# Performance work log

Measured on AMD Instinct MI355X. Metric: run time of the kernel, lower is better.

The kernel has to match this reference:

```python
import jax, jax.numpy as jnp
import numpy as np

H, DH, DM = 8, 128, 1024          # n_head, d_head, d_model (n_head*d_head == d_model)
SLEN, BSZ = 256, 64               # slen <= 256 forced by pi0[:, :l]
SCALE = 1.0 / DH ** 0.5
LN_EPS = 1e-5


def setup_inputs() -> dict:
    key = jax.random.key(0)
    k0, k1, k2, k3 = jax.random.split(key, 4)
    h = jax.random.normal(k0, (SLEN, BSZ, DM), jnp.float32)
    W_qkv = jax.random.normal(k1, (H * 4 * DH, DM), jnp.float32) * (DM ** -0.5)
    W_o = jax.random.normal(k2, (DM, H * DH), jnp.float32) * ((H * DH) ** -0.5)
    pi0 = jax.random.uniform(k3, (H, 256), jnp.float32)
    ln_gamma = jnp.ones((DM,), jnp.float32)
    ln_beta = jnp.zeros((DM,), jnp.float32)
    return {"h": h, "W_qkv": W_qkv, "W_o": W_o, "pi0": pi0,
            "ln_gamma": ln_gamma, "ln_beta": ln_beta}


def _phi(x):
    # elu(x)+1 feature map, then L1-normalize over the feature dim
    x = jax.nn.elu(x) + 1.0
    return x / jnp.sum(x, axis=-1, keepdims=True)


def _causal_linear_attn(q, k, v):
    # fast_weight_sum: out_t = sum_{s<=t} (q_t . k_s) v_s  (zero initial fast weights)
    # q,k,v: [b,h,l,d]
    l = q.shape[2]
    scores = jnp.einsum('bhld,bhsd->bhls', q, k)
    mask = jnp.tril(jnp.ones((l, l), dtype=bool))
    scores = jnp.where(mask, scores, jnp.zeros((), scores.dtype))
    return jnp.einsum('bhls,bhsd->bhld', scores, v)


def reference(h, W_qkv, W_o, pi0, ln_gamma, ln_beta):
    l, b, _ = h.shape
    # qkv projection: [l,b,H,4*DH] -> q, k1, k2, v (update_mode='rbf2keys')
    qkv = jnp.einsum('lbm,nm->lbn', h, W_qkv).reshape(l, b, H, 4 * DH)
    q, k1, k2, v = jnp.split(qkv, 4, axis=-1)
    # permute to [b, H, l, d]
    q = _phi(jnp.transpose(q, (1, 2, 0, 3)))
    k1 = _phi(jnp.transpose(k1, (1, 2, 0, 3)))
    k2 = _phi(jnp.transpose(k2, (1, 2, 0, 3)))
    v = jnp.transpose(v, (1, 2, 0, 3))
    # two fast-weight sums (skip_attn_normalization=True path)
    lo1 = _causal_linear_attn(q, k1, v)
    lo2 = _causal_linear_attn(q, k2, v)
    pi = jnp.clip(pi0, 0.0, 1.0)[None, :, :l, None]          # [1,H,l,1]
    layer_out = SCALE * (lo1 * pi + lo2 * (1.0 - pi))         # [b,H,l,d]
    # [b,H,l,d] -> [l,b,H*d]
    layer_out = jnp.transpose(layer_out, (2, 0, 1, 3)).reshape(l, b, H * DH)
    attn_out = jnp.einsum('lbn,mn->lbm', layer_out, W_o)
    # post-LN residual (pre_lnorm=False, dropout=0)
    x = h + attn_out
    mu = jnp.mean(x, axis=-1, keepdims=True)
    var = jnp.mean((x - mu) ** 2, axis=-1, keepdims=True)
    return ln_gamma * (x - mu) / jnp.sqrt(var + LN_EPS) + ln_beta
```

## Files before the change

kernel.cpp:

```cpp
#include <hip/hip_runtime.h>

#define H_     8
#define DM_    1024
#define NQKV_  4096
#define ROWS_  16384
#define PAIRS_ 512
#define SCALE_ 0.08838834764831845f
#define LN_EPS_ 1e-5f

typedef __attribute__((ext_vector_type(8))) short short8;
typedef __attribute__((ext_vector_type(4))) float floatx4;

__device__ __forceinline__ float b2f(unsigned short u) {
  union { unsigned int i; float f; } v; v.i = ((unsigned int)u) << 16; return v.f;
}
__device__ __forceinline__ unsigned short f2b(float f) {
  union { unsigned int i; float f; } v; v.f = f;
  unsigned int b = v.i;
  b += 0x7FFFu + ((b >> 16) & 1u);
  return (unsigned short)(b >> 16);
}

__device__ __forceinline__ void stage_async(const unsigned short* __restrict__ g,
                                            size_t ld, unsigned short* s, int tid) {
#pragma unroll
  for (int p = 0; p < 4; ++p) {
    int idx = p * 256 + tid;
    int r = idx >> 3, j = idx & 7;
    int cg = j ^ (r & 7);
    __builtin_amdgcn_global_load_lds(
        (const __attribute__((address_space(1))) unsigned int*)(g + (size_t)r * ld + cg * 8),
        (__attribute__((address_space(3))) unsigned int*)(s + (size_t)idx * 8),
        16, 0, 0);
  }
}
__device__ __forceinline__ void stage_h(const unsigned short* __restrict__ g,
                                        size_t o0, size_t o1,
                                        unsigned short* s, int lo0, int lo1) {
  __builtin_amdgcn_global_load_lds(
      (const __attribute__((address_space(1))) unsigned int*)(g + o0),
      (__attribute__((address_space(3))) unsigned int*)(s + lo0), 16, 0, 0);
  __builtin_amdgcn_global_load_lds(
      (const __attribute__((address_space(1))) unsigned int*)(g + o1),
      (__attribute__((address_space(3))) unsigned int*)(s + lo1), 16, 0, 0);
}
__device__ __forceinline__ short8 lds_frag(const unsigned short* s, int row, int cg) {
  return *(const short8*)(s + row * 64 + ((cg ^ (row & 7)) << 3));
}

__global__ __launch_bounds__(256) void cvt_all(const float* __restrict__ h,
                                               const float* __restrict__ wq,
                                               const float* __restrict__ wo,
                                               unsigned short* __restrict__ hb,
                                               unsigned short* __restrict__ wqb,
                                               unsigned short* __restrict__ wob) {
  int i = blockIdx.x * 256 + threadIdx.x;
  const float* src; unsigned short* dst; int off;
  if (i < 2097152)      { src = h;  dst = hb;  off = i; }
  else if (i < 2621440) { src = wq; dst = wqb; off = i - 2097152; }
  else                  { src = wo; dst = wob; off = i - 2621440; }
  const float4* s4 = (const float4*)(src + (size_t)off * 8);
  float4 v0 = s4[0], v1 = s4[1];
  union { short8 v; unsigned short u[8]; } pk;
  pk.u[0] = f2b(v0.x); pk.u[1] = f2b(v0.y); pk.u[2] = f2b(v0.z); pk.u[3] = f2b(v0.w);
  pk.u[4] = f2b(v1.x); pk.u[5] = f2b(v1.y); pk.u[6] = f2b(v1.z); pk.u[7] = f2b(v1.w);
  *(short8*)(dst + (size_t)off * 8) = pk.v;
}

__global__ __launch_bounds__(512, 2) void qkv_gemm(const unsigned short* __restrict__ A,
                                                   const unsigned short* __restrict__ B,
                                                   unsigned short* __restrict__ QKV) {
  __shared__ alignas(16) unsigned short Sh[65536];
  int tid = threadIdx.x;
  int lane = tid & 63, wid = tid >> 6;
  int wm = wid >> 2, wn = wid & 3;
  int quad = lane >> 4, l16 = lane & 15;
  int s7 = l16 & 7;

  int bid = blockIdx.y * 16 + blockIdx.x;
  int swz = (bid & 7) * 128 + (bid >> 3);
  int bx = swz & 15, by = swz >> 4;
  int n0 = bx * 256, hh = bx >> 1, part0 = (bx & 1) * 2, bb = by;

  const unsigned short* Ab = A + (size_t)bb * DM_;
  const size_t lda = (size_t)64 * DM_;
  const unsigned short* AbH = Ab + (size_t)128 * lda;
  const unsigned short* Bb = B + (size_t)n0 * DM_;
  const unsigned short* BbH = Bb + (size_t)128 * DM_;

  int r0 = tid >> 3, jj = tid & 7;
  int cg = jj ^ (r0 & 7);
  size_t oA0 = (size_t)r0 * lda + cg * 8;
  size_t oA1 = (size_t)(r0 + 64) * lda + cg * 8;
  size_t oB0 = (size_t)r0 * DM_ + cg * 8;
  size_t oB1 = (size_t)(r0 + 64) * DM_ + cg * 8;
  int lo0 = tid * 8, lo1 = 4096 + tid * 8;

  floatx4 acc[8][4];
#pragma unroll
  for (int i = 0; i < 8; ++i)
#pragma unroll
    for (int j = 0; j < 4; ++j)
#pragma unroll
      for (int r = 0; r < 4; ++r) acc[i][j][r] = 0.f;

  stage_h(Ab,        oA0, oA1, Sh,         lo0, lo1);
  stage_h(AbH,       oA0, oA1, Sh + 8192,  lo0, lo1);
  stage_h(Bb,        oB0, oB1, Sh + 16384, lo0, lo1);
  stage_h(BbH,       oB0, oB1, Sh + 24576, lo0, lo1);
  stage_h(Ab + 64,   oA0, oA1, Sh + 32768, lo0, lo1);
  stage_h(AbH + 64,  oA0, oA1, Sh + 40960, lo0, lo1);
  asm volatile("s_waitcnt vmcnt(4)" ::: "memory");
  __builtin_amdgcn_s_barrier();

#define TILE_BODY(T, BUF, OBUF)                                                \
  {                                                                            \
    unsigned short* SB = (BUF) + 16384;                                        \
    const unsigned short* aA0 = (BUF) + (wm * 128 + l16) * 64 + ((0 ^ (quad ^ s7)) ? 0 : 0) + ((quad ^ s7) << 3); \
    const unsigned short* aA1 = (BUF) + (wm * 128 + l16) * 64 + (((4 + quad) ^ s7) << 3); \
    const unsigned short* bA0 = SB + (wn * 64 + l16) * 64 + ((quad ^ s7) << 3);\
    const unsigned short* bA1 = SB + (wn * 64 + l16) * 64 + (((4 + quad) ^ s7) << 3); \
    short8 a[8], b[4];                                                         \
                   \
    if ((T) < 15) {                                                            \
      size_t kn = (size_t)((T) + 1) * 64;                                      \
      stage_h(Bb + kn,  oB0, oB1, (OBUF) + 16384, lo0, lo1);                   \
      stage_h(BbH + kn, oB0, oB1, (OBUF) + 24576, lo0, lo1);                   \
    }                                                                          \
    _Pragma("unroll")                                                          \
    for (int mt = 0; mt < 4; ++mt) {                                           \
      a[mt * 2 + 0] = *(const short8*)(aA0 + mt * 1024);                       \
      a[mt * 2 + 1] = *(const short8*)(aA1 + mt * 1024);                       \
    }                                                                          \
    _Pragma("unroll")                                                          \
    for (int nt = 0; nt < 2; ++nt) {                                           \
      b[nt * 2 + 0] = *(const short8*)(bA0 + nt * 1024);                       \
      b[nt * 2 + 1] = *(const short8*)(bA1 + nt * 1024);                       \
    }                                                                          \
    __builtin_amdgcn_sched_barrier(0);                                         \
    __builtin_amdgcn_s_barrier();                                              \
    __builtin_amdgcn_s_setprio(1);                                             \
    _Pragma("unroll")                                                          \
    for (int kk = 0; kk < 2; ++kk)                                             \
      _Pragma("unroll")                                                        \
      for (int m = 0; m < 4; ++m)                                              \
        _Pragma("unroll")                                                      \
        for (int n = 0; n < 2; ++n)                                            \
          acc[m][n] = __builtin_amdgcn_mfma_f32_16x16x32_bf16(a[m * 2 + kk], b[n * 2 + kk], acc[m][n], 0, 0, 0); \
    __builtin_amdgcn_s_setprio(0);                                             \
    __builtin_amdgcn_s_barrier();                                              \
                                                 \
    _Pragma("unroll")                                                          \
    for (int nt = 0; nt < 2; ++nt) {                                           \
      b[nt * 2 + 0] = *(const short8*)(bA0 + 2048 + nt * 1024);                \
      b[nt * 2 + 1] = *(const short8*)(bA1 + 2048 + nt * 1024);                \
    }                                                                          \
    __builtin_amdgcn_sched_barrier(0);                                         \
    __builtin_amdgcn_s_barrier();                                              \
    __builtin_amdgcn_s_setprio(1);                                             \
    _Pragma("unroll")                                                          \
    for (int kk = 0; kk < 2; ++kk)                                             \
      _Pragma("unroll")                                                        \
      for (int m = 0; m < 4; ++m)                                              \
        _Pragma("unroll")                                                      \
        for (int n = 0; n < 2; ++n)                                            \
          acc[m][2 + n] = __builtin_amdgcn_mfma_f32_16x16x32_bf16(a[m * 2 + kk], b[n * 2 + kk], acc[m][2 + n], 0, 0, 0); \
    __builtin_amdgcn_s_setprio(0);                                             \
    __builtin_amdgcn_s_barrier();                                              \
                                       \
    _Pragma("unroll")                                                          \
    for (int mt = 0; mt < 4; ++mt) {                                           \
      a[mt * 2 + 0] = *(const short8*)(aA0 + 4096 + mt * 1024);                \
      a[mt * 2 + 1] = *(const short8*)(aA1 + 4096 + mt * 1024);                \
    }                                                                          \
    __builtin_amdgcn_sched_barrier(0);                                         \
    __builtin_amdgcn_s_barrier();                                              \
    __builtin_amdgcn_s_setprio(1);                                             \
    _Pragma("unroll")                                                          \
    for (int kk = 0; kk < 2; ++kk)                                             \
      _Pragma("unroll")                                                        \
      for (int m = 0; m < 4; ++m)                                              \
        _Pragma("unroll")                                                      \
        for (int n = 0; n < 2; ++n)                                            \
          acc[4 + m][2 + n] = __builtin_amdgcn_mfma_f32_16x16x32_bf16(a[m * 2 + kk], b[n * 2 + kk], acc[4 + m][2 + n], 0, 0, 0); \
    __builtin_amdgcn_s_setprio(0);                                             \
    __builtin_amdgcn_s_barrier();                                              \
                \
    if ((T) < 14) {                                                            \
      size_t kt2 = (size_t)((T) + 2) * 64;                                     \
      stage_h(Ab + kt2,  oA0, oA1, (BUF),        lo0, lo1);                    \
      stage_h(AbH + kt2, oA0, oA1, (BUF) + 8192, lo0, lo1);                    \
    }                                                                          \
    _Pragma("unroll")                                                          \
    for (int nt = 0; nt < 2; ++nt) {                                           \
      b[nt * 2 + 0] = *(const short8*)(bA0 + nt * 1024);                       \
      b[nt * 2 + 1] = *(const short8*)(bA1 + nt * 1024);                       \
    }                                                                          \
    __builtin_amdgcn_sched_barrier(0);                                         \
    __builtin_amdgcn_s_barrier();                                              \
    __builtin_amdgcn_s_setprio(1);                                             \
    _Pragma("unroll")                                                          \
    for (int kk = 0; kk < 2; ++kk)                                             \
      _Pragma("unroll")                                                        \
      for (int m = 0; m < 4; ++m)                                              \
        _Pragma("unroll")                                                      \
        for (int n = 0; n < 2; ++n)                                            \
          acc[4 + m][n] = __builtin_amdgcn_mfma_f32_16x16x32_bf16(a[m * 2 + kk], b[n * 2 + kk], acc[4 + m][n], 0, 0, 0); \
    __builtin_amdgcn_s_setprio(0);                                             \
    if ((T) < 14) { asm volatile("s_waitcnt vmcnt(4)" ::: "memory"); }         \
    else          { asm volatile("s_waitcnt vmcnt(0)" ::: "memory"); }         \
    __builtin_amdgcn_s_barrier();                                              \
  }

  for (int t = 0; t < 16; t += 2) {
    TILE_BODY(t,     Sh,         Sh + 32768)
    TILE_BODY(t + 1, Sh + 32768, Sh)
  }
#undef TILE_BODY

  __syncthreads();
  bool isV = (part0 + (wn >> 1)) == 3;
  float* Pf = (float*)Sh;
  float rsum[8][4];
  float inv[8][4];
  if (!isV) {
#pragma unroll
    for (int mt = 0; mt < 8; ++mt)
#pragma unroll
      for (int r = 0; r < 4; ++r) rsum[mt][r] = 0.f;
#pragma unroll
    for (int mt = 0; mt < 8; ++mt)
#pragma unroll
      for (int nt = 0; nt < 4; ++nt)
#pragma unroll
        for (int r = 0; r < 4; ++r) {
          float x = acc[mt][nt][r];
          float f = x > 0.f ? x + 1.f : __expf(x);
          acc[mt][nt][r] = f;
          rsum[mt][r] += f;
        }
#pragma unroll
    for (int off = 1; off < 16; off <<= 1)
#pragma unroll
      for (int mt = 0; mt < 8; ++mt)
#pragma unroll
        for (int r = 0; r < 4; ++r)
          rsum[mt][r] += __shfl_xor(rsum[mt][r], off);
    if (l16 == 0) {
#pragma unroll
      for (int mt = 0; mt < 8; ++mt)
#pragma unroll
        for (int r = 0; r < 4; ++r)
          Pf[(wm * 128 + mt * 16 + quad * 4 + r) * 4 + wn] = rsum[mt][r];
    }
  }
  __syncthreads();
  if (!isV) {
#pragma unroll
    for (int mt = 0; mt < 8; ++mt)
#pragma unroll
      for (int r = 0; r < 4; ++r)
        inv[mt][r] = 1.f / (rsum[mt][r] + Pf[(wm * 128 + mt * 16 + quad * 4 + r) * 4 + (wn ^ 1)]);
  }
  __syncthreads();

#pragma unroll
  for (int h = 0; h < 2; ++h) {
    int part = part0 + h;
    if ((wn >> 1) == h) {
      if (part < 3) {
#pragma unroll
        for (int mt = 0; mt < 8; ++mt)
#pragma unroll
          for (int nt = 0; nt < 4; ++nt)
#pragma unroll
            for (int r = 0; r < 4; ++r) {
              int row = wm * 128 + mt * 16 + quad * 4 + r;
              int col = (wn & 1) * 64 + nt * 16 + l16;
              Sh[row * 136 + col] = f2b(acc[mt][nt][r] * inv[mt][r]);
            }
      } else {
#pragma unroll
        for (int mt = 0; mt < 8; ++mt)
#pragma unroll
          for (int nt = 0; nt < 4; ++nt)
#pragma unroll
            for (int r = 0; r < 4; ++r) {
              int d = (wn & 1) * 64 + nt * 16 + l16;
              int l = wm * 128 + mt * 16 + quad * 4 + r;
              Sh[d * 264 + l] = f2b(acc[mt][nt][r]);
            }
      }
    }
    __syncthreads();
    if (part < 3) {
      unsigned short* P = QKV + (size_t)part * 16777216 + (size_t)(bb * 8 + hh) * 32768;
      int c = tid & 15, g = tid >> 4;
#pragma unroll
      for (int j = 0; j < 8; ++j) {
        int row = j * 32 + g;
        *(short8*)(P + (size_t)row * 128 + c * 8) = *(const short8*)(Sh + row * 136 + c * 8);
      }
    } else {
      unsigned short* Vt = QKV + (size_t)3 * 16777216 + (size_t)(bb * 8 + hh) * 32768;
      int cg2 = tid & 31, g = tid >> 5;
#pragma unroll
      for (int j = 0; j < 8; ++j) {
        int d = j * 16 + g;
        *(short8*)(Vt + (size_t)d * 256 + cg2 * 8) = *(const short8*)(Sh + d * 264 + cg2 * 8);
      }
    }
    __syncthreads();
  }
}

__global__ __launch_bounds__(256) void scores_kernel(const unsigned short* __restrict__ QKV,
                                                     const float* __restrict__ pi0,
                                                     unsigned short* __restrict__ S) {
  __shared__ alignas(16) unsigned short Sh[24576];
  __shared__ float pis[128];
  unsigned short* As  = Sh;
  unsigned short* Bs1 = Sh + 8192;
  unsigned short* Bs2 = Sh + 16384;
  int p = blockIdx.z;
  int hh = p & 7;
  int tid = threadIdx.x;
  int lane = tid & 63, wid = tid >> 6;
  int wm = wid >> 1, wn = wid & 1;
  int quad = lane >> 4, l16 = lane & 15;
  int tix = blockIdx.x;
  int m0 = (tix >= 1) ? 128 : 0;
  int n0 = (tix == 2) ? 128 : 0;
  if (tid < 128) {
    float pv = pi0[hh * 256 + m0 + tid];
    pis[tid] = fminf(fmaxf(pv, 0.f), 1.f);
  }
  const unsigned short* Qb  = QKV + (size_t)p * 32768 + (size_t)m0 * 128;
  const unsigned short* K1b = QKV + 16777216     + (size_t)p * 32768 + (size_t)n0 * 128;
  const unsigned short* K2b = QKV + 2 * 16777216 + (size_t)p * 32768 + (size_t)n0 * 128;

  floatx4 acc1[4][4], acc2[4][4];
#pragma unroll
  for (int i = 0; i < 4; ++i)
#pragma unroll
    for (int j = 0; j < 4; ++j)
#pragma unroll
      for (int r = 0; r < 4; ++r) { acc1[i][j][r] = 0.f; acc2[i][j][r] = 0.f; }

  for (int kt = 0; kt < 128; kt += 64) {
    stage_async(Qb + kt, 128, As, tid);
    stage_async(K1b + kt, 128, Bs1, tid);
    stage_async(K2b + kt, 128, Bs2, tid);
    __syncthreads();
#pragma unroll
    for (int kk = 0; kk < 2; ++kk) {
      short8 af[4], b1[4], b2v[4];
#pragma unroll
      for (int mt = 0; mt < 4; ++mt)
        af[mt] = lds_frag(As, wm * 64 + mt * 16 + l16, kk * 4 + quad);
#pragma unroll
      for (int nt = 0; nt < 4; ++nt) {
        b1[nt]  = lds_frag(Bs1, wn * 64 + nt * 16 + l16, kk * 4 + quad);
        b2v[nt] = lds_frag(Bs2, wn * 64 + nt * 16 + l16, kk * 4 + quad);
      }
#pragma unroll
      for (int mt = 0; mt < 4; ++mt)
#pragma unroll
        for (int nt = 0; nt < 4; ++nt) {
          acc1[mt][nt] = __builtin_amdgcn_mfma_f32_16x16x32_bf16(af[mt], b1[nt],  acc1[mt][nt], 0, 0, 0);
          acc2[mt][nt] = __builtin_amdgcn_mfma_f32_16x16x32_bf16(af[mt], b2v[nt], acc2[mt][nt], 0, 0, 0);
        }
    }
    __syncthreads();
  }
#pragma unroll
  for (int mt = 0; mt < 4; ++mt)
#pragma unroll
    for (int nt = 0; nt < 4; ++nt)
#pragma unroll
      for (int r = 0; r < 4; ++r) {
        int tl = wm * 64 + mt * 16 + quad * 4 + r;
        int sl = wn * 64 + nt * 16 + l16;
        float pv = pis[tl];
        float v = (n0 + sl <= m0 + tl) ? (pv * acc1[mt][nt][r] + (1.f - pv) * acc2[mt][nt][r]) : 0.f;
        Sh[tl * 136 + sl] = f2b(v);
      }
  __syncthreads();
  int c = tid & 15, g = tid >> 4;
#pragma unroll
  for (int j = 0; j < 8; ++j) {
    int r = j * 16 + g;
    size_t gb = (size_t)p * 65536 + (size_t)(m0 + r) * 256 + n0 + c * 8;
    *(short8*)(S + gb) = *(const short8*)(Sh + r * 136 + c * 8);
  }
}

__global__ __launch_bounds__(256, 4) void pv_kernel(const unsigned short* __restrict__ S,
                                                    const unsigned short* __restrict__ Vt,
                                                    unsigned short* __restrict__ LO) {
  __shared__ alignas(16) unsigned short Sh[17408];
  unsigned short* As = Sh;
  unsigned short* Bs = Sh + 8192;
  int p = blockIdx.z;
  int b = p >> 3, hh = p & 7;
  int tid = threadIdx.x;
  int lane = tid & 63, wid = tid >> 6;
  int wm = wid >> 1, wn = wid & 1;
  int quad = lane >> 4, l16 = lane & 15;
  int m0 = blockIdx.y * 128;
  int kEnd = (blockIdx.y == 0) ? 128 : 256;
  const unsigned short* Ab = S  + (size_t)p * 65536 + (size_t)m0 * 256;
  const unsigned short* Bb = Vt + (size_t)p * 32768;

  floatx4 acc[4][4];
#pragma unroll
  for (int i = 0; i < 4; ++i)
#pragma unroll
    for (int j = 0; j < 4; ++j)
#pragma unroll
      for (int r = 0; r < 4; ++r) acc[i][j][r] = 0.f;

  for (int kt = 0; kt < kEnd; kt += 64) {
    stage_async(Ab + kt, 256, As, tid);
    stage_async(Bb + kt, 256, Bs, tid);
    __syncthreads();
#pragma unroll
    for (int kk = 0; kk < 2; ++kk) {
      short8 af[4], bfv[4];
#pragma unroll
      for (int mt = 0; mt < 4; ++mt)
        af[mt] = lds_frag(As, wm * 64 + mt * 16 + l16, kk * 4 + quad);
#pragma unroll
      for (int nt = 0; nt < 4; ++nt)
        bfv[nt] = lds_frag(Bs, wn * 64 + nt * 16 + l16, kk * 4 + quad);
#pragma unroll
      for (int mt = 0; mt < 4; ++mt)
#pragma unroll
        for (int nt = 0; nt < 4; ++nt)
          acc[mt][nt] = __builtin_amdgcn_mfma_f32_16x16x32_bf16(af[mt], bfv[nt], acc[mt][nt], 0, 0, 0);
    }
    __syncthreads();
  }
#pragma unroll
  for (int mt = 0; mt < 4; ++mt)
#pragma unroll
    for (int nt = 0; nt < 4; ++nt)
#pragma unroll
      for (int r = 0; r < 4; ++r) {
        int tl = wm * 64 + mt * 16 + quad * 4 + r;
        int d = wn * 64 + nt * 16 + l16;
        Sh[tl * 136 + d] = f2b(SCALE_ * acc[mt][nt][r]);
      }
  __syncthreads();
  int c = tid & 15, g = tid >> 4;
#pragma unroll
  for (int j = 0; j < 8; ++j) {
    int r = j * 16 + g;
    int t = m0 + r;
    size_t gb = ((size_t)t * 64 + b) * 1024 + hh * 128 + c * 8;
    *(short8*)(LO + gb) = *(const short8*)(Sh + r * 136 + c * 8);
  }
}

__global__ __launch_bounds__(256, 4) void wo_gemm(const unsigned short* __restrict__ A,
                                                  const unsigned short* __restrict__ B,
                                                  const float* __restrict__ hin,
                                                  float* __restrict__ X) {
  __shared__ alignas(16) unsigned short As[128 * 64], Bs[128 * 64];
  int tid = threadIdx.x;
  int lane = tid & 63, wid = tid >> 6;
  int wm = wid >> 1, wn = wid & 1;
  int quad = lane >> 4, l16 = lane & 15;
  int m0 = blockIdx.y * 128, n0 = blockIdx.x * 128;
  const unsigned short* Ab = A + (size_t)m0 * DM_;
  const unsigned short* Bb = B + (size_t)n0 * DM_;

  floatx4 acc[4][4];
#pragma unroll
  for (int i = 0; i < 4; ++i)
#pragma unroll
    for (int j = 0; j < 4; ++j)
#pragma unroll
      for (int r = 0; r < 4; ++r) acc[i][j][r] = 0.f;

  for (int kt = 0; kt < DM_; kt += 64) {
    stage_async(Ab + kt, DM_, As, tid);
    stage_async(Bb + kt, DM_, Bs, tid);
    __syncthreads();
#pragma unroll
    for (int kk = 0; kk < 2; ++kk) {
      short8 af[4], bfv[4];
#pragma unroll
      for (int mt = 0; mt < 4; ++mt)
        af[mt] = lds_frag(As, wm * 64 + mt * 16 + l16, kk * 4 + quad);
#pragma unroll
      for (int nt = 0; nt < 4; ++nt)
        bfv[nt] = lds_frag(Bs, wn * 64 + nt * 16 + l16, kk * 4 + quad);
#pragma unroll
      for (int mt = 0; mt < 4; ++mt)
#pragma unroll
        for (int nt = 0; nt < 4; ++nt)
          acc[mt][nt] = __builtin_amdgcn_mfma_f32_16x16x32_bf16(af[mt], bfv[nt], acc[mt][nt], 0, 0, 0);
    }
    __syncthreads();
  }
#pragma unroll
  for (int mt = 0; mt < 4; ++mt)
#pragma unroll
    for (int nt = 0; nt < 4; ++nt)
#pragma unroll
      for (int r = 0; r < 4; ++r) {
        int row = m0 + wm * 64 + mt * 16 + quad * 4 + r;
        int col = n0 + wn * 64 + nt * 16 + l16;
        size_t idx = (size_t)row * DM_ + col;
        X[idx] = acc[mt][nt][r] + hin[idx];
      }
}

__global__ __launch_bounds__(256) void ln_kernel(float* __restrict__ X,
                                                 const float* __restrict__ gamma,
                                                 const float* __restrict__ beta) {
  int row = blockIdx.x;
  int tid = threadIdx.x;
  float* x = X + (size_t)row * DM_;
  float4 v = *(const float4*)(x + tid * 4);
  float s  = v.x + v.y + v.z + v.w;
  float ss = v.x * v.x + v.y * v.y + v.z * v.z + v.w * v.w;
#pragma unroll
  for (int off = 32; off; off >>= 1) {
    s  += __shfl_down(s, off);
    ss += __shfl_down(ss, off);
  }
  __shared__ float rs[4], rss[4];
  int wv = tid >> 6, lane = tid & 63;
  if (lane == 0) { rs[wv] = s; rss[wv] = ss; }
  __syncthreads();
  float St  = rs[0] + rs[1] + rs[2] + rs[3];
  float SSt = rss[0] + rss[1] + rss[2] + rss[3];
  float mu = St * (1.f / DM_);
  float var = SSt * (1.f / DM_) - mu * mu;
  float rstd = rsqrtf(var + LN_EPS_);
  float4 o;
#pragma unroll
  for (int j = 0; j < 4; ++j) {
    int c = tid * 4 + j;
    (&o.x)[j] = gamma[c] * ((&v.x)[j] - mu) * rstd + beta[c];
  }
  *(float4*)(x + tid * 4) = o;
}

extern "C" void kernel_launch(void* const* d_in, const int* in_sizes, int n_in,
                              void* d_out, int out_size, void* d_ws, size_t ws_size,
                              hipStream_t stream) {
  const float* h     = (const float*)d_in[0];
  const float* Wqkv  = (const float*)d_in[1];
  const float* Wo    = (const float*)d_in[2];
  const float* pi0   = (const float*)d_in[3];
  const float* gamma = (const float*)d_in[4];
  const float* beta  = (const float*)d_in[5];
  char* ws = (char*)d_ws;

  unsigned short* QKV   = (unsigned short*)ws;
  unsigned short* Sbuf  = (unsigned short*)(ws + 134217728ull);
  unsigned short* hb    = (unsigned short*)(ws + 134217728ull);
  unsigned short* Wqkvb = (unsigned short*)(ws + 167772160ull);
  unsigned short* Wob   = (unsigned short*)(ws + 201326592ull);
  unsigned short* LO    = (unsigned short*)ws;
  float* X = (float*)d_out;

  dim3 blk(256);
  cvt_all<<<dim3(10752), blk, 0, stream>>>(h, Wqkv, Wo, hb, Wqkvb, Wob);
  qkv_gemm<<<dim3(16, 64, 1), dim3(512), 0, stream>>>(hb, Wqkvb, QKV);
  scores_kernel<<<dim3(3, 1, PAIRS_), blk, 0, stream>>>(QKV, pi0, Sbuf);
  pv_kernel<<<dim3(1, 2, PAIRS_), blk, 0, stream>>>(Sbuf, QKV + (size_t)3 * 16777216, LO);
  wo_gemm<<<dim3(DM_ / 128, ROWS_ / 128, 1), blk, 0, stream>>>(LO, Wob, h, X);
  ln_kernel<<<dim3(ROWS_, 1, 1), blk, 0, stream>>>(X, gamma, beta);
}
```

Baseline: 438.7 us.

## Fuse scores and PV kernels into one attention kernel keeping scores in LDS

Replaces the separate scores and PV kernels with one attn_kernel. Each block computes the mixed, causally masked score panels for its query tile and keeps them in swizzled shared memory, then multiplies them by V without writing S to global memory. This removes the global round trip for the score matrix and one launch. The cost is more shared memory per block (80 KB), serial work in the second query tile, and only 2 blocks per query pair. The qkv_gemm launch bound is also relaxed to one block per SM.

After: 466.0 us. +6.2%, slower.

```diff
diff --git a/kernel.cpp b/kernel.cpp
--- a/kernel.cpp
+++ b/kernel.cpp
@@ -67,7 +67,7 @@
   *(short8*)(dst + (size_t)off * 8) = pk.v;
 }
 
-__global__ __launch_bounds__(512, 2) void qkv_gemm(const unsigned short* __restrict__ A,
+__global__ __launch_bounds__(512, 1) void qkv_gemm(const unsigned short* __restrict__ A,
                                                    const unsigned short* __restrict__ B,
                                                    unsigned short* __restrict__ QKV) {
   __shared__ alignas(16) unsigned short Sh[65536];
@@ -116,7 +116,7 @@
 #define TILE_BODY(T, BUF, OBUF)                                                \
   {                                                                            \
     unsigned short* SB = (BUF) + 16384;                                        \
-    const unsigned short* aA0 = (BUF) + (wm * 128 + l16) * 64 + ((0 ^ (quad ^ s7)) ? 0 : 0) + ((quad ^ s7) << 3); \
+    const unsigned short* aA0 = (BUF) + (wm * 128 + l16) * 64 + ((quad ^ s7) << 3); \
     const unsigned short* aA1 = (BUF) + (wm * 128 + l16) * 64 + (((4 + quad) ^ s7) << 3); \
     const unsigned short* bA0 = SB + (wn * 64 + l16) * 64 + ((quad ^ s7) << 3);\
     const unsigned short* bA1 = SB + (wn * 64 + l16) * 64 + (((4 + quad) ^ s7) << 3); \
@@ -314,103 +314,82 @@
   }
 }
 
-__global__ __launch_bounds__(256) void scores_kernel(const unsigned short* __restrict__ QKV,
-                                                     const float* __restrict__ pi0,
-                                                     unsigned short* __restrict__ S) {
-  __shared__ alignas(16) unsigned short Sh[24576];
-  __shared__ float pis[128];
-  unsigned short* As  = Sh;
-  unsigned short* Bs1 = Sh + 8192;
-  unsigned short* Bs2 = Sh + 16384;
+__global__ __launch_bounds__(256, 2) void attn_kernel(const unsigned short* __restrict__ QKV,
+                                                      const float* __restrict__ pi0,
+                                                      unsigned short* __restrict__ LO) {
+  __shared__ alignas(16) unsigned short Stg[24576];
+  __shared__ alignas(16) unsigned short Span[16384];
+  unsigned short* As  = Stg;
+  unsigned short* Bs1 = Stg + 8192;
+  unsigned short* Bs2 = Stg + 16384;
   int p = blockIdx.z;
-  int hh = p & 7;
+  int b = p >> 3, hh = p & 7;
+  int mi = blockIdx.x;
+  int m0 = mi * 128;
   int tid = threadIdx.x;
   int lane = tid & 63, wid = tid >> 6;
   int wm = wid >> 1, wn = wid & 1;
   int quad = lane >> 4, l16 = lane & 15;
-  int tix = blockIdx.x;
-  int m0 = (tix >= 1) ? 128 : 0;
-  int n0 = (tix == 2) ? 128 : 0;
-  if (tid < 128) {
-    float pv = pi0[hh * 256 + m0 + tid];
-    pis[tid] = fminf(fmaxf(pv, 0.f), 1.f);
-  }
-  const unsigned short* Qb  = QKV + (size_t)p * 32768 + (size_t)m0 * 128;
-  const unsigned short* K1b = QKV + 16777216     + (size_t)p * 32768 + (size_t)n0 * 128;
-  const unsigned short* K2b = QKV + 2 * 16777216 + (size_t)p * 32768 + (size_t)n0 * 128;
-
-  floatx4 acc1[4][4], acc2[4][4];
-#pragma unroll
-  for (int i = 0; i < 4; ++i)
-#pragma unroll
-    for (int j = 0; j < 4; ++j)
-#pragma unroll
-      for (int r = 0; r < 4; ++r) { acc1[i][j][r] = 0.f; acc2[i][j][r] = 0.f; }
-
-  for (int kt = 0; kt < 128; kt += 64) {
-    stage_async(Qb + kt, 128, As, tid);
-    stage_async(K1b + kt, 128, Bs1, tid);
-    stage_async(K2b + kt, 128, Bs2, tid);
-    __syncthreads();
-#pragma unroll
-    for (int kk = 0; kk < 2; ++kk) {
-      short8 af[4], b1[4], b2v[4];
-#pragma unroll
-      for (int mt = 0; mt < 4; ++mt)
-        af[mt] = lds_frag(As, wm * 64 + mt * 16 + l16, kk * 4 + quad);
-#pragma unroll
-      for (int nt = 0; nt < 4; ++nt) {
-        b1[nt]  = lds_frag(Bs1, wn * 64 + nt * 16 + l16, kk * 4 + quad);
-        b2v[nt] = lds_frag(Bs2, wn * 64 + nt * 16 + l16, kk * 4 + quad);
-      }
-#pragma unroll
-      for (int mt = 0; mt < 4; ++mt)
+
+  const unsigned short* Qb = QKV + (size_t)p * 32768 + (size_t)m0 * 128;
+
+  for (int nb = 0; nb <= mi; ++nb) {
+    int n0 = nb * 128;
+    const unsigned short* K1b = QKV + 16777216     + (size_t)p * 32768 + (size_t)n0 * 128;
+    const unsigned short* K2b = QKV + 2 * 16777216 + (size_t)p * 32768 + (size_t)n0 * 128;
+
+    floatx4 acc1[4][4], acc2[4][4];
+#pragma unroll
+    for (int i = 0; i < 4; ++i)
+#pragma unroll
+      for (int j = 0; j < 4; ++j)
+#pragma unroll
+        for (int r = 0; r < 4; ++r) { acc1[i][j][r] = 0.f; acc2[i][j][r] = 0.f; }
+
+    for (int kt = 0; kt < 128; kt += 64) {
+      stage_async(Qb + kt, 128, As, tid);
+      stage_async(K1b + kt, 128, Bs1, tid);
+      stage_async(K2b + kt, 128, Bs2, tid);
+      __syncthreads();
+#pragma unroll
+      for (int kk = 0; kk < 2; ++kk) {
+        short8 af[4], b1[4], b2v[4];
+#pragma unroll
+        for (int mt = 0; mt < 4; ++mt)
+          af[mt] = lds_frag(As, wm * 64 + mt * 16 + l16, kk * 4 + quad);
 #pragma unroll
         for (int nt = 0; nt < 4; ++nt) {
-          acc1[mt][nt] = __builtin_amdgcn_mfma_f32_16x16x32_bf16(af[mt], b1[nt],  acc1[mt][nt], 0, 0, 0);
-          acc2[mt][nt] = __builtin_amdgcn_mfma_f32_16x16x32_bf16(af[mt], b2v[nt], acc2[mt][nt], 0, 0, 0);
+          b1[nt]  = lds_frag(Bs1, wn * 64 + nt * 16 + l16, kk * 4 + quad);
+          b2v[nt] = lds_frag(Bs2, wn * 64 + nt * 16 + l16, kk * 4 + quad);
         }
+#pragma unroll
+        for (int mt = 0; mt < 4; ++mt)
+#pragma unroll
+          for (int nt = 0; nt < 4; ++nt) {
+            acc1[mt][nt] = __builtin_amdgcn_mfma_f32_16x16x32_bf16(af[mt], b1[nt],  acc1[mt][nt], 0, 0, 0);
+            acc2[mt][nt] = __builtin_amdgcn_mfma_f32_16x16x32_bf16(af[mt], b2v[nt], acc2[mt][nt], 0, 0, 0);
+          }
+      }
+      __syncthreads();
     }
-    __syncthreads();
-  }
-#pragma unroll
-  for (int mt = 0; mt < 4; ++mt)
-#pragma unroll
-    for (int nt = 0; nt < 4; ++nt)
+    bool diag = (nb == mi);
+    unsigned short* Pan = Span + (size_t)(nb * 2 + wn) * 8192;
+#pragma unroll
+    for (int mt = 0; mt < 4; ++mt)
 #pragma unroll
       for (int r = 0; r < 4; ++r) {
         int tl = wm * 64 + mt * 16 + quad * 4 + r;
-        int sl = wn * 64 + nt * 16 + l16;
-        float pv = pis[tl];
-        float v = (n0 + sl <= m0 + tl) ? (pv * acc1[mt][nt][r] + (1.f - pv) * acc2[mt][nt][r]) : 0.f;
-        Sh[tl * 136 + sl] = f2b(v);
-      }
-  __syncthreads();
-  int c = tid & 15, g = tid >> 4;
-#pragma unroll
-  for (int j = 0; j < 8; ++j) {
-    int r = j * 16 + g;
-    size_t gb = (size_t)p * 65536 + (size_t)(m0 + r) * 256 + n0 + c * 8;
-    *(short8*)(S + gb) = *(const short8*)(Sh + r * 136 + c * 8);
-  }
-}
-
-__global__ __launch_bounds__(256, 4) void pv_kernel(const unsigned short* __restrict__ S,
-                                                    const unsigned short* __restrict__ Vt,
-                                                    unsigned short* __restrict__ LO) {
-  __shared__ alignas(16) unsigned short Sh[17408];
-  unsigned short* As = Sh;
-  unsigned short* Bs = Sh + 8192;
-  int p = blockIdx.z;
-  int b = p >> 3, hh = p & 7;
-  int tid = threadIdx.x;
-  int lane = tid & 63, wid = tid >> 6;
-  int wm = wid >> 1, wn = wid & 1;
-  int quad = lane >> 4, l16 = lane & 15;
-  int m0 = blockIdx.y * 128;
-  int kEnd = (blockIdx.y == 0) ? 128 : 256;
-  const unsigned short* Ab = S  + (size_t)p * 65536 + (size_t)m0 * 256;
-  const unsigned short* Bb = Vt + (size_t)p * 32768;
+        float pv = pi0[hh * 256 + m0 + tl];
+        pv = fminf(fmaxf(pv, 0.f), 1.f);
+#pragma unroll
+        for (int nt = 0; nt < 4; ++nt) {
+          int slc = nt * 16 + l16;
+          float v = pv * acc1[mt][nt][r] + (1.f - pv) * acc2[mt][nt][r];
+          if (diag && (n0 + wn * 64 + slc > m0 + tl)) v = 0.f;
+          Pan[tl * 64 + (((slc >> 3) ^ (tl & 7)) << 3) + (slc & 7)] = f2b(v);
+        }
+      }
+  }
 
   floatx4 acc[4][4];
 #pragma unroll
@@ -420,19 +399,21 @@
 #pragma unroll
       for (int r = 0; r < 4; ++r) acc[i][j][r] = 0.f;
 
+  int kEnd = m0 + 128;
+  const unsigned short* Vb = QKV + (size_t)3 * 16777216 + (size_t)p * 32768;
   for (int kt = 0; kt < kEnd; kt += 64) {
-    stage_async(Ab + kt, 256, As, tid);
-    stage_async(Bb + kt, 256, Bs, tid);
+    stage_async(Vb + kt, 256, Bs1, tid);
     __syncthreads();
+    const unsigned short* Ap = Span + (size_t)(kt >> 6) * 8192;
 #pragma unroll
     for (int kk = 0; kk < 2; ++kk) {
       short8 af[4], bfv[4];
 #pragma unroll
       for (int mt = 0; mt < 4; ++mt)
-        af[mt] = lds_frag(As, wm * 64 + mt * 16 + l16, kk * 4 + quad);
+        af[mt] = lds_frag(Ap, wm * 64 + mt * 16 + l16, kk * 4 + quad);
 #pragma unroll
       for (int nt = 0; nt < 4; ++nt)
-        bfv[nt] = lds_frag(Bs, wn * 64 + nt * 16 + l16, kk * 4 + quad);
+        bfv[nt] = lds_frag(Bs1, wn * 64 + nt * 16 + l16, kk * 4 + quad);
 #pragma unroll
       for (int mt = 0; mt < 4; ++mt)
 #pragma unroll
@@ -441,6 +422,7 @@
     }
     __syncthreads();
   }
+
 #pragma unroll
   for (int mt = 0; mt < 4; ++mt)
 #pragma unroll
@@ -449,7 +431,9 @@
       for (int r = 0; r < 4; ++r) {
         int tl = wm * 64 + mt * 16 + quad * 4 + r;
         int d = wn * 64 + nt * 16 + l16;
-        Sh[tl * 136 + d] = f2b(SCALE_ * acc[mt][nt][r]);
+        int dc = d & 63;
+        Span[(size_t)(d >> 6) * 8192 + tl * 64 + (((dc >> 3) ^ (tl & 7)) << 3) + (dc & 7)] =
+            f2b(SCALE_ * acc[mt][nt][r]);
       }
   __syncthreads();
   int c = tid & 15, g = tid >> 4;
@@ -457,8 +441,9 @@
   for (int j = 0; j < 8; ++j) {
     int r = j * 16 + g;
     int t = m0 + r;
+    short8 val = *(const short8*)(Span + (size_t)(c >> 3) * 8192 + r * 64 + (((c & 7) ^ (r & 7)) << 3));
     size_t gb = ((size_t)t * 64 + b) * 1024 + hh * 128 + c * 8;
-    *(short8*)(LO + gb) = *(const short8*)(Sh + r * 136 + c * 8);
+    *(short8*)(LO + gb) = val;
   }
 }
 
@@ -561,18 +546,16 @@
   char* ws = (char*)d_ws;
 
   unsigned short* QKV   = (unsigned short*)ws;
-  unsigned short* Sbuf  = (unsigned short*)(ws + 134217728ull);
   unsigned short* hb    = (unsigned short*)(ws + 134217728ull);
   unsigned short* Wqkvb = (unsigned short*)(ws + 167772160ull);
   unsigned short* Wob   = (unsigned short*)(ws + 201326592ull);
-  unsigned short* LO    = (unsigned short*)ws;
+  unsigned short* LO    = (unsigned short*)(ws + 134217728ull);
   float* X = (float*)d_out;
 
   dim3 blk(256);
   cvt_all<<<dim3(10752), blk, 0, stream>>>(h, Wqkv, Wo, hb, Wqkvb, Wob);
   qkv_gemm<<<dim3(16, 64, 1), dim3(512), 0, stream>>>(hb, Wqkvb, QKV);
-  scores_kernel<<<dim3(3, 1, PAIRS_), blk, 0, stream>>>(QKV, pi0, Sbuf);
-  pv_kernel<<<dim3(1, 2, PAIRS_), blk, 0, stream>>>(Sbuf, QKV + (size_t)3 * 16777216, LO);
+  attn_kernel<<<dim3(2, 1, PAIRS_), blk, 0, stream>>>(QKV, pi0, LO);
   wo_gemm<<<dim3(DM_ / 128, ROWS_ / 128, 1), blk, 0, stream>>>(LO, Wob, h, X);
   ln_kernel<<<dim3(ROWS_, 1, 1), blk, 0, stream>>>(X, gamma, beta);
 }
```

## Reuse pipelined 256x256 qkv GEMM tile for Wo projection, fuse residual into LN

Applied to the files above, without the earlier changes.

The Wo GEMM now reuses the double-buffered, swizzled 256x256 TILE_BODY pipeline from the QKV GEMM instead of a simple 128x128 synchronous loop. It writes a bf16 attention output through an LDS-staged coalesced store. The residual add moves into a new ln_res kernel that reads bf16 attn plus fp32 h. This is meant to raise GEMM efficiency and cut fp32 X write/read traffic, at the cost of rounding attn_out to bf16 before the residual. qkv_gemm launch bounds also change from 2 to 1 block per CU.

Result: faster. 423.9 us (-3.4%).

```diff
diff --git a/kernel.cpp b/kernel.cpp
--- a/kernel.cpp
+++ b/kernel.cpp
@@ -9,6 +9,7 @@
 #define LN_EPS_ 1e-5f
 
 typedef __attribute__((ext_vector_type(8))) short short8;
+typedef __attribute__((ext_vector_type(4))) short short4v;
 typedef __attribute__((ext_vector_type(4))) float floatx4;
 
 __device__ __forceinline__ float b2f(unsigned short u) {
@@ -67,56 +68,10 @@
   *(short8*)(dst + (size_t)off * 8) = pk.v;
 }
 
-__global__ __launch_bounds__(512, 2) void qkv_gemm(const unsigned short* __restrict__ A,
-                                                   const unsigned short* __restrict__ B,
-                                                   unsigned short* __restrict__ QKV) {
-  __shared__ alignas(16) unsigned short Sh[65536];
-  int tid = threadIdx.x;
-  int lane = tid & 63, wid = tid >> 6;
-  int wm = wid >> 2, wn = wid & 3;
-  int quad = lane >> 4, l16 = lane & 15;
-  int s7 = l16 & 7;
-
-  int bid = blockIdx.y * 16 + blockIdx.x;
-  int swz = (bid & 7) * 128 + (bid >> 3);
-  int bx = swz & 15, by = swz >> 4;
-  int n0 = bx * 256, hh = bx >> 1, part0 = (bx & 1) * 2, bb = by;
-
-  const unsigned short* Ab = A + (size_t)bb * DM_;
-  const size_t lda = (size_t)64 * DM_;
-  const unsigned short* AbH = Ab + (size_t)128 * lda;
-  const unsigned short* Bb = B + (size_t)n0 * DM_;
-  const unsigned short* BbH = Bb + (size_t)128 * DM_;
-
-  int r0 = tid >> 3, jj = tid & 7;
-  int cg = jj ^ (r0 & 7);
-  size_t oA0 = (size_t)r0 * lda + cg * 8;
-  size_t oA1 = (size_t)(r0 + 64) * lda + cg * 8;
-  size_t oB0 = (size_t)r0 * DM_ + cg * 8;
-  size_t oB1 = (size_t)(r0 + 64) * DM_ + cg * 8;
-  int lo0 = tid * 8, lo1 = 4096 + tid * 8;
-
-  floatx4 acc[8][4];
-#pragma unroll
-  for (int i = 0; i < 8; ++i)
-#pragma unroll
-    for (int j = 0; j < 4; ++j)
-#pragma unroll
-      for (int r = 0; r < 4; ++r) acc[i][j][r] = 0.f;
-
-  stage_h(Ab,        oA0, oA1, Sh,         lo0, lo1);
-  stage_h(AbH,       oA0, oA1, Sh + 8192,  lo0, lo1);
-  stage_h(Bb,        oB0, oB1, Sh + 16384, lo0, lo1);
-  stage_h(BbH,       oB0, oB1, Sh + 24576, lo0, lo1);
-  stage_h(Ab + 64,   oA0, oA1, Sh + 32768, lo0, lo1);
-  stage_h(AbH + 64,  oA0, oA1, Sh + 40960, lo0, lo1);
-  asm volatile("s_waitcnt vmcnt(4)" ::: "memory");
-  __builtin_amdgcn_s_barrier();
-
 #define TILE_BODY(T, BUF, OBUF)                                                \
   {                                                                            \
     unsigned short* SB = (BUF) + 16384;                                        \
-    const unsigned short* aA0 = (BUF) + (wm * 128 + l16) * 64 + ((0 ^ (quad ^ s7)) ? 0 : 0) + ((quad ^ s7) << 3); \
+    const unsigned short* aA0 = (BUF) + (wm * 128 + l16) * 64 + ((quad ^ s7) << 3); \
     const unsigned short* aA1 = (BUF) + (wm * 128 + l16) * 64 + (((4 + quad) ^ s7) << 3); \
     const unsigned short* bA0 = SB + (wn * 64 + l16) * 64 + ((quad ^ s7) << 3);\
     const unsigned short* bA1 = SB + (wn * 64 + l16) * 64 + (((4 + quad) ^ s7) << 3); \
@@ -124,8 +79,8 @@
                    \
     if ((T) < 15) {                                                            \
       size_t kn = (size_t)((T) + 1) * 64;                                      \
-      stage_h(Bb + kn,  oB0, oB1, (OBUF) + 16384, lo0, lo1);                   \
-      stage_h(BbH + kn, oB0, oB1, (OBUF) + 24576, lo0, lo1);                   \
+      stage_h(BbP + kn,  oB0, oB1, (OBUF) + 16384, lo0, lo1);                  \
+      stage_h(BbHP + kn, oB0, oB1, (OBUF) + 24576, lo0, lo1);                  \
     }                                                                          \
     _Pragma("unroll")                                                          \
     for (int mt = 0; mt < 4; ++mt) {                                           \
@@ -188,8 +143,8 @@
                 \
     if ((T) < 14) {                                                            \
       size_t kt2 = (size_t)((T) + 2) * 64;                                     \
-      stage_h(Ab + kt2,  oA0, oA1, (BUF),        lo0, lo1);                    \
-      stage_h(AbH + kt2, oA0, oA1, (BUF) + 8192, lo0, lo1);                    \
+      stage_h(AbP + kt2,  oA0, oA1, (BUF),        lo0, lo1);                   \
+      stage_h(AbHP + kt2, oA0, oA1, (BUF) + 8192, lo0, lo1);                   \
     }                                                                          \
     _Pragma("unroll")                                                          \
     for (int nt = 0; nt < 2; ++nt) {                                           \
@@ -212,11 +167,56 @@
     __builtin_amdgcn_s_barrier();                                              \
   }
 
+__global__ __launch_bounds__(512, 1) void qkv_gemm(const unsigned short* __restrict__ A,
+                                                   const unsigned short* __restrict__ B,
+                                                   unsigned short* __restrict__ QKV) {
+  __shared__ alignas(16) unsigned short Sh[65536];
+  int tid = threadIdx.x;
+  int lane = tid & 63, wid = tid >> 6;
+  int wm = wid >> 2, wn = wid & 3;
+  int quad = lane >> 4, l16 = lane & 15;
+  int s7 = l16 & 7;
+
+  int bid = blockIdx.y * 16 + blockIdx.x;
+  int swz = (bid & 7) * 128 + (bid >> 3);
+  int bx = swz & 15, by = swz >> 4;
+  int n0 = bx * 256, hh = bx >> 1, part0 = (bx & 1) * 2, bb = by;
+
+  const unsigned short* AbP = A + (size_t)bb * DM_;
+  const size_t lda = (size_t)64 * DM_;
+  const unsigned short* AbHP = AbP + (size_t)128 * lda;
+  const unsigned short* BbP = B + (size_t)n0 * DM_;
+  const unsigned short* BbHP = BbP + (size_t)128 * DM_;
+
+  int r0 = tid >> 3, jj = tid & 7;
+  int cg = jj ^ (r0 & 7);
+  size_t oA0 = (size_t)r0 * lda + cg * 8;
+  size_t oA1 = (size_t)(r0 + 64) * lda + cg * 8;
+  size_t oB0 = (size_t)r0 * DM_ + cg * 8;
+  size_t oB1 = (size_t)(r0 + 64) * DM_ + cg * 8;
+  int lo0 = tid * 8, lo1 = 4096 + tid * 8;
+
+  floatx4 acc[8][4];
+#pragma unroll
+  for (int i = 0; i < 8; ++i)
+#pragma unroll
+    for (int j = 0; j < 4; ++j)
+#pragma unroll
+      for (int r = 0; r < 4; ++r) acc[i][j][r] = 0.f;
+
+  stage_h(AbP,        oA0, oA1, Sh,         lo0, lo1);
+  stage_h(AbHP,       oA0, oA1, Sh + 8192,  lo0, lo1);
+  stage_h(BbP,        oB0, oB1, Sh + 16384, lo0, lo1);
+  stage_h(BbHP,       oB0, oB1, Sh + 24576, lo0, lo1);
+  stage_h(AbP + 64,   oA0, oA1, Sh + 32768, lo0, lo1);
+  stage_h(AbHP + 64,  oA0, oA1, Sh + 40960, lo0, lo1);
+  asm volatile("s_waitcnt vmcnt(4)" ::: "memory");
+  __builtin_amdgcn_s_barrier();
+
   for (int t = 0; t < 16; t += 2) {
     TILE_BODY(t,     Sh,         Sh + 32768)
     TILE_BODY(t + 1, Sh + 32768, Sh)
   }
-#undef TILE_BODY
 
   __syncthreads();
   bool isV = (part0 + (wn >> 1)) == 3;
@@ -265,9 +265,9 @@
   __syncthreads();
 
 #pragma unroll
-  for (int h = 0; h < 2; ++h) {
-    int part = part0 + h;
-    if ((wn >> 1) == h) {
+  for (int hq = 0; hq < 2; ++hq) {
+    int part = part0 + hq;
+    if ((wn >> 1) == hq) {
       if (part < 3) {
 #pragma unroll
         for (int mt = 0; mt < 8; ++mt)
@@ -462,70 +462,100 @@
   }
 }
 
-__global__ __launch_bounds__(256, 4) void wo_gemm(const unsigned short* __restrict__ A,
+__global__ __launch_bounds__(512, 1) void wo_gemm(const unsigned short* __restrict__ A,
                                                   const unsigned short* __restrict__ B,
-                                                  const float* __restrict__ hin,
-                                                  float* __restrict__ X) {
-  __shared__ alignas(16) unsigned short As[128 * 64], Bs[128 * 64];
+                                                  unsigned short* __restrict__ attn) {
+  __shared__ alignas(16) unsigned short Sh[65536];
   int tid = threadIdx.x;
   int lane = tid & 63, wid = tid >> 6;
-  int wm = wid >> 1, wn = wid & 1;
+  int wm = wid >> 2, wn = wid & 3;
   int quad = lane >> 4, l16 = lane & 15;
-  int m0 = blockIdx.y * 128, n0 = blockIdx.x * 128;
-  const unsigned short* Ab = A + (size_t)m0 * DM_;
-  const unsigned short* Bb = B + (size_t)n0 * DM_;
-
-  floatx4 acc[4][4];
-#pragma unroll
-  for (int i = 0; i < 4; ++i)
+  int s7 = l16 & 7;
+
+  int bid = blockIdx.y * 4 + blockIdx.x;
+  int swz = (bid & 7) * 32 + (bid >> 3);
+  int bx = swz & 3, by = swz >> 2;
+  int n0 = bx * 256, m0 = by * 256;
+
+  const unsigned short* AbP = A + (size_t)m0 * DM_;
+  const unsigned short* AbHP = AbP + (size_t)128 * DM_;
+  const unsigned short* BbP = B + (size_t)n0 * DM_;
+  const unsigned short* BbHP = BbP + (size_t)128 * DM_;
+
+  int r0 = tid >> 3, jj = tid & 7;
+  int cg = jj ^ (r0 & 7);
+  size_t oA0 = (size_t)r0 * DM_ + cg * 8;
+  size_t oA1 = (size_t)(r0 + 64) * DM_ + cg * 8;
+  size_t oB0 = oA0, oB1 = oA1;
+  int lo0 = tid * 8, lo1 = 4096 + tid * 8;
+
+  floatx4 acc[8][4];
+#pragma unroll
+  for (int i = 0; i < 8; ++i)
 #pragma unroll
     for (int j = 0; j < 4; ++j)
 #pragma unroll
       for (int r = 0; r < 4; ++r) acc[i][j][r] = 0.f;
 
-  for (int kt = 0; kt < DM_; kt += 64) {
-    stage_async(Ab + kt, DM_, As, tid);
-    stage_async(Bb + kt, DM_, Bs, tid);
-    __syncthreads();
-#pragma unroll
-    for (int kk = 0; kk < 2; ++kk) {
-      short8 af[4], bfv[4];
-#pragma unroll
-      for (int mt = 0; mt < 4; ++mt)
-        af[mt] = lds_frag(As, wm * 64 + mt * 16 + l16, kk * 4 + quad);
-#pragma unroll
-      for (int nt = 0; nt < 4; ++nt)
-        bfv[nt] = lds_frag(Bs, wn * 64 + nt * 16 + l16, kk * 4 + quad);
-#pragma unroll
-      for (int mt = 0; mt < 4; ++mt)
+  stage_h(AbP,        oA0, oA1, Sh,         lo0, lo1);
+  stage_h(AbHP,       oA0, oA1, Sh + 8192,  lo0, lo1);
+  stage_h(BbP,        oB0, oB1, Sh + 16384, lo0, lo1);
+  stage_h(BbHP,       oB0, oB1, Sh + 24576, lo0, lo1);
+  stage_h(AbP + 64,   oA0, oA1, Sh + 32768, lo0, lo1);
+  stage_h(AbHP + 64,  oA0, oA1, Sh + 40960, lo0, lo1);
+  asm volatile("s_waitcnt vmcnt(4)" ::: "memory");
+  __builtin_amdgcn_s_barrier();
+
+  for (int t = 0; t < 16; t += 2) {
+    TILE_BODY(t,     Sh,         Sh + 32768)
+    TILE_BODY(t + 1, Sh + 32768, Sh)
+  }
+
+  __syncthreads();
+#pragma unroll
+  for (int hq = 0; hq < 2; ++hq) {
+    if ((wn >> 1) == hq) {
+#pragma unroll
+      for (int mt = 0; mt < 8; ++mt)
 #pragma unroll
         for (int nt = 0; nt < 4; ++nt)
-          acc[mt][nt] = __builtin_amdgcn_mfma_f32_16x16x32_bf16(af[mt], bfv[nt], acc[mt][nt], 0, 0, 0);
+#pragma unroll
+          for (int r = 0; r < 4; ++r) {
+            int row = wm * 128 + mt * 16 + quad * 4 + r;
+            int col = (wn & 1) * 64 + nt * 16 + l16;
+            Sh[row * 136 + col] = f2b(acc[mt][nt][r]);
+          }
     }
     __syncthreads();
-  }
-#pragma unroll
-  for (int mt = 0; mt < 4; ++mt)
-#pragma unroll
-    for (int nt = 0; nt < 4; ++nt)
-#pragma unroll
-      for (int r = 0; r < 4; ++r) {
-        int row = m0 + wm * 64 + mt * 16 + quad * 4 + r;
-        int col = n0 + wn * 64 + nt * 16 + l16;
-        size_t idx = (size_t)row * DM_ + col;
-        X[idx] = acc[mt][nt][r] + hin[idx];
-      }
-}
-
-__global__ __launch_bounds__(256) void ln_kernel(float* __restrict__ X,
-                                                 const float* __restrict__ gamma,
-                                                 const float* __restrict__ beta) {
+    int c = tid & 15, g = tid >> 4;
+#pragma unroll
+    for (int j = 0; j < 8; ++j) {
+      int row = j * 32 + g;
+      *(short8*)(attn + (size_t)(m0 + row) * DM_ + n0 + hq * 128 + c * 8) =
+          *(const short8*)(Sh + row * 136 + c * 8);
+    }
+    __syncthreads();
+  }
+}
+
+__global__ __launch_bounds__(256) void ln_res(const unsigned short* __restrict__ attn,
+                                              const float* __restrict__ hin,
+                                              const float* __restrict__ gamma,
+                                              const float* __restrict__ beta,
+                                              float* __restrict__ out) {
   int row = blockIdx.x;
   int tid = threadIdx.x;
-  float* x = X + (size_t)row * DM_;
-  float4 v = *(const float4*)(x + tid * 4);
-  float s  = v.x + v.y + v.z + v.w;
-  float ss = v.x * v.x + v.y * v.y + v.z * v.z + v.w * v.w;
+  const unsigned short* ap = attn + (size_t)row * DM_ + tid * 4;
+  const float* hp = hin + (size_t)row * DM_ + tid * 4;
+  short4v av = *(const short4v*)ap;
+  float4 hv = *(const float4*)hp;
+  float x[4];
+  x[0] = hv.x + b2f((unsigned short)av[0]);
+  x[1] = hv.y + b2f((unsigned short)av[1]);
+  x[2] = hv.z + b2f((unsigned short)av[2]);
+  x[3] = hv.w + b2f((unsigned short)av[3]);
+  float s  = x[0] + x[1] + x[2] + x[3];
+  float ss = x[0] * x[0] + x[1] * x[1] + x[2] * x[2] + x[3] * x[3];
 #pragma unroll
   for (int off = 32; off; off >>= 1) {
     s  += __shfl_down(s, off);
@@ -544,9 +574,9 @@
 #pragma unroll
   for (int j = 0; j < 4; ++j) {
     int c = tid * 4 + j;
-    (&o.x)[j] = gamma[c] * ((&v.x)[j] - mu) * rstd + beta[c];
-  }
-  *(float4*)(x + tid * 4) = o;
+    (&o.x)[j] = gamma[c] * (x[j] - mu) * rstd + beta[c];
+  }
+  *(float4*)(out + (size_t)row * DM_ + tid * 4) = o;
 }
 
 extern "C" void kernel_launch(void* const* d_in, const int* in_sizes, int n_in,
@@ -566,6 +596,7 @@
   unsigned short* Wqkvb = (unsigned short*)(ws + 167772160ull);
   unsigned short* Wob   = (unsigned short*)(ws + 201326592ull);
   unsigned short* LO    = (unsigned short*)ws;
+  unsigned short* attn  = (unsigned short*)(ws + 134217728ull);
   float* X = (float*)d_out;
 
   dim3 blk(256);
@@ -573,6 +604,6 @@
   qkv_gemm<<<dim3(16, 64, 1), dim3(512), 0, stream>>>(hb, Wqkvb, QKV);
   scores_kernel<<<dim3(3, 1, PAIRS_), blk, 0, stream>>>(QKV, pi0, Sbuf);
   pv_kernel<<<dim3(1, 2, PAIRS_), blk, 0, stream>>>(Sbuf, QKV + (size_t)3 * 16777216, LO);
-  wo_gemm<<<dim3(DM_ / 128, ROWS_ / 128, 1), blk, 0, stream>>>(LO, Wob, h, X);
-  ln_kernel<<<dim3(ROWS_, 1, 1), blk, 0, stream>>>(X, gamma, beta);
-}
+  wo_gemm<<<dim3(4, 64, 1), dim3(512), 0, stream>>>(LO, Wob, attn);
+  ln_res<<<dim3(ROWS_, 1, 1), blk, 0, stream>>>(attn, h, gamma, beta, X);
+}
```
